# Kernel tuning notes

Measured on AMD Instinct MI355X. Metric: run time of the kernel, lower is better.

## Reference

```python
import jax, jax.numpy as jnp
import numpy as np

B, VH, VL, EP = 4, 130, 120, 256
DIN, DEP, D, H, NL = 256, 128, 512, 16, 8
HID = 4 * D

def _pe(x, base=1000.0):
    # sinusoidal positional encoding (base=1000 as in the module)
    L, Dm = x.shape[-2], x.shape[-1]
    pos = jnp.arange(L, dtype=jnp.float32)
    ch = jnp.arange(Dm, dtype=jnp.float32)
    ang = pos[:, None] / (base ** (2.0 * ch / ch[-1]))[None]
    enc = jnp.where(ch % 2 == 0, jnp.sin(ang), jnp.cos(ang))
    return x + enc

def _ln(x, g, b):
    m = x.mean(-1, keepdims=True)
    v = ((x - m) ** 2).mean(-1, keepdims=True)
    return (x - m) / jnp.sqrt(v + 1e-5) * g + b

def _gmha(x, rots, trans, mask_bias, qkv_w, out_w, out_b, g, b, r_s, d_s):
    # ESM3 geometric multi-head attention (algorithm 6)
    xn = _ln(x, g, b)
    qkv = (xn @ qkv_w.T).reshape(x.shape[0], x.shape[1], 5, H, 3)  # [B,L,5,H,3]
    qkv = jnp.einsum('brid,brfhd->brfhi', rots, qkv)               # rotate into global frame
    Qr, Kr, Qd, Kd, V = (qkv[..., f, :, :] for f in range(5))
    scale = 3.0 ** -0.5
    Ar = jnp.einsum('bihd,bjhd->bijh', Qr, Kr) * jax.nn.softplus(r_s) * scale
    qd = Qd + trans[:, :, None, :]
    kd = Kd + trans[:, :, None, :]
    dist = jnp.linalg.norm(qd[:, :, None] - kd[:, None], axis=-1)  # [B,i,j,H]
    logits = Ar - dist * jax.nn.softplus(d_s) * scale + mask_bias[..., None]
    A = jax.nn.softmax(logits, axis=2)
    o = jnp.einsum('bijh,bjhd->bihd', A, V)
    o = jnp.einsum('brji,brhj->brhi', rots, o)                     # rotate back (R^T)
    return o.reshape(x.shape[0], x.shape[1], H * 3) @ out_w.T + out_b

def _swiglu(x, g, b, w12, w3):
    # SwiGLU transition (dropout is identity in eval)
    h = _ln(x, g, b) @ w12.T
    a, v = jnp.split(h, 2, axis=-1)
    return (jax.nn.silu(a) * v) @ w3.T

def _forward(vh_x, vl_x, vh_rots, vh_trans, vl_rots, vl_trans, ep_feats, ep_rots, ep_trans,
             vh_emb_w, vl_emb_w, tgt_emb_w, qkv_w, out_w, out_b, ln_g, ln_b, r_scale, d_scale,
             ln2_g, ln2_b, w12, w3, out_vh_w, out_vh_gate_w, out_vh_gate_b,
             out_vl_w, out_vl_gate_w, out_vl_gate_b, vh_mask, vl_mask, ep_mask):
    emb = jnp.concatenate([_pe(vh_x @ vh_emb_w.T), _pe(vl_x @ vl_emb_w.T), ep_feats @ tgt_emb_w.T], axis=1)
    rots = jnp.concatenate([vh_rots, vl_rots, ep_rots], axis=1)
    trans = jnp.concatenate([vh_trans, vl_trans, ep_trans], axis=1)
    mask = jnp.concatenate([vh_mask, vl_mask, ep_mask], axis=1)
    mask_bias = jnp.where(mask[:, :, None] | mask[:, None, :], -1e9, 0.0)
    for i in range(NL):
        emb = emb + _gmha(emb, rots, trans, mask_bias, qkv_w[i], out_w[i], out_b[i],
                          ln_g[i], ln_b[i], r_scale[i], d_scale[i])
        emb = emb + _swiglu(emb, ln2_g[i], ln2_b[i], w12[i], w3[i])
    vh_e, vl_e = emb[:, :VH], emb[:, VH:VH + VL]
    vh_upd = (vh_e @ out_vh_w.T) * jax.nn.sigmoid(vh_e @ out_vh_gate_w.T + out_vh_gate_b)
    vl_upd = (vl_e @ out_vl_w.T) * jax.nn.sigmoid(vl_e @ out_vl_gate_w.T + out_vl_gate_b)
    vh_out = jnp.where(~vh_mask[..., None], vh_x + vh_upd, vh_x)
    vl_out = jnp.where(~vl_mask[..., None], vl_x + vl_upd, vl_x)
    return vh_out, vl_out

def setup_inputs():
    key = jax.random.key(0)
    ks = iter(jax.random.split(key, 40))
    s = 0.02
    return dict(
        vh_x=jax.random.normal(next(ks), (B, VH, DIN)),
        vl_x=jax.random.normal(next(ks), (B, VL, DIN)),
        vh_rots=jax.random.normal(next(ks), (B, VH, 3, 3)),
        vh_trans=jax.random.normal(next(ks), (B, VH, 3)),
        vl_rots=jax.random.normal(next(ks), (B, VL, 3, 3)),
        vl_trans=jax.random.normal(next(ks), (B, VL, 3)),
        ep_feats=jax.random.normal(next(ks), (B, EP, DEP)),
        ep_rots=jax.random.normal(next(ks), (B, EP, 3, 3)),
        ep_trans=jax.random.normal(next(ks), (B, EP, 3)),
        vh_mask=jnp.zeros((B, VH), dtype=bool),
        vl_mask=jnp.zeros((B, VL), dtype=bool),
        ep_mask=jax.random.randint(next(ks), (B, EP), 0, 2).astype(bool),
        vh_emb_w=jax.random.normal(next(ks), (D, DIN)) * s,
        vl_emb_w=jax.random.normal(next(ks), (D, DIN)) * s,
        tgt_emb_w=jax.random.normal(next(ks), (D, DEP)) * s,
        qkv_w=jax.random.normal(next(ks), (NL, H * 15, D)) * s,
        out_w=jax.random.normal(next(ks), (NL, D, H * 3)) * s,
        out_b=jnp.zeros((NL, D)),
        ln_g=jnp.ones((NL, D)), ln_b=jnp.zeros((NL, D)),
        r_scale=jnp.zeros((NL, H)), d_scale=jnp.zeros((NL, H)),
        ln2_g=jnp.ones((NL, D)), ln2_b=jnp.zeros((NL, D)),
        w12=jax.random.normal(next(ks), (NL, 2 * HID, D)) * s,
        w3=jax.random.normal(next(ks), (NL, D, HID)) * s,
        out_vh_w=jax.random.normal(next(ks), (DIN, D)) * s,
        out_vh_gate_w=jax.random.normal(next(ks), (DIN, D)) * s,
        out_vh_gate_b=jnp.full((DIN,), -2.0),
        out_vl_w=jax.random.normal(next(ks), (DIN, D)) * s,
        out_vl_gate_w=jax.random.normal(next(ks), (DIN, D)) * s,
        out_vl_gate_b=jnp.full((DIN,), -2.0),
    )

def reference(vh_x, vl_x, vh_rots, vh_trans, vl_rots, vl_trans, ep_feats, ep_rots, ep_trans,
              vh_mask, vl_mask, ep_mask,
              vh_emb_w, vl_emb_w, tgt_emb_w, qkv_w, out_w, out_b, ln_g, ln_b, r_scale, d_scale,
              ln2_g, ln2_b, w12, w3, out_vh_w, out_vh_gate_w, out_vh_gate_b,
              out_vl_w, out_vl_gate_w, out_vl_gate_b):
    return _forward(vh_x, vl_x, vh_rots, vh_trans, vl_rots, vl_trans, ep_feats, ep_rots, ep_trans,
                    vh_emb_w, vl_emb_w, tgt_emb_w, qkv_w, out_w, out_b, ln_g, ln_b, r_scale, d_scale,
                    ln2_g, ln2_b, w12, w3, out_vh_w, out_vh_gate_w, out_vh_gate_b,
                    out_vl_w, out_vl_gate_w, out_vl_gate_b, vh_mask, vl_mask, ep_mask)
```

## Files before the change

### kernel.cpp

```cpp
#include <hip/hip_runtime.h>
#include <hip/hip_bf16.h>
#include <math.h>
#include <stdint.h>

#define B_ 4
#define VH_ 130
#define VL_ 120
#define EP_ 256
#define R_ 506
#define RP_ 512
#define DIN_ 256
#define DEP_ 128
#define D_ 512
#define H_ 16
#define NL_ 8
#define HID_ 2048

#define MODE_STORE 0
#define MODE_ADD_BIAS 1

typedef _Float16 half8 __attribute__((ext_vector_type(8)));
typedef float f32x4 __attribute__((ext_vector_type(4)));

#define ASYNC16(ldsdst, gsrc)                                                  \
  __builtin_amdgcn_global_load_lds(                                            \
      (const __attribute__((address_space(1))) unsigned int*)(gsrc),           \
      (__attribute__((address_space(3))) unsigned int*)(ldsdst), 16, 0, 0)

__global__ __launch_bounds__(256) void gemm16sw_kernel(
    const _Float16* __restrict__ A, const _Float16* __restrict__ Wa,
    const _Float16* __restrict__ Wv, _Float16* __restrict__ Gh,
    int M, int K) {
  __shared__ _Float16 Al[4][4096];
  __shared__ _Float16 Ba[4][2048];
  __shared__ _Float16 Bv[4][2048];

  const int t = threadIdx.x;
  const int nbm = (M + 127) >> 7;
  const int nwg = gridDim.x;
  int bid = blockIdx.x;
  if ((nwg & 7) == 0) {
    int q = nwg >> 3;
    bid = (bid & 7) * q + (bid >> 3);
  }
  const int bm = bid % nbm, bn = bid / nbm;
  const int lane = t & 63;
  const int w = t >> 6;
  const int wm = w >> 1, wn = w & 1;

  const int r0 = t >> 2;
  const int cp = t & 3;
  const int gc = cp ^ ((r0 >> 1) & 3);
  int gr0 = bm * 128 + r0;       if (gr0 >= M) gr0 = M - 1;
  int gr1 = bm * 128 + 64 + r0;  if (gr1 >= M) gr1 = M - 1;
  const int gcol = bn * 64 + r0;
  const _Float16* pA0 = A + (size_t)gr0 * K + gc * 8;
  const _Float16* pA1 = A + (size_t)gr1 * K + gc * 8;
  const _Float16* pBa = Wa + (size_t)gcol * K + gc * 8;
  const _Float16* pBv = Wv + (size_t)gcol * K + gc * 8;

#define STAGE(buf, kt)                                                         \
  do {                                                                         \
    ASYNC16(&Al[buf][t * 8], pA0 + (size_t)(kt) * 32);                         \
    ASYNC16(&Al[buf][2048 + t * 8], pA1 + (size_t)(kt) * 32);                  \
    ASYNC16(&Ba[buf][t * 8], pBa + (size_t)(kt) * 32);                         \
    ASYNC16(&Bv[buf][t * 8], pBv + (size_t)(kt) * 32);                         \
  } while (0)

  f32x4 aca[4][2], acv[4][2];
#pragma unroll
  for (int i = 0; i < 4; i++)
#pragma unroll
    for (int j = 0; j < 2; j++) {
      aca[i][j] = (f32x4){0.f, 0.f, 0.f, 0.f};
      acv[i][j] = (f32x4){0.f, 0.f, 0.f, 0.f};
    }

  const int nt = K >> 5;
  STAGE(0, 0); STAGE(1, 1); STAGE(2, 2);

  const int rl = lane & 15;
  const int ca = (lane >> 4) ^ ((rl >> 1) & 3);
  for (int kt = 0; kt < nt; ++kt) {
    if (kt < nt - 2)       asm volatile("s_waitcnt vmcnt(8)" ::: "memory");
    else if (kt == nt - 2) asm volatile("s_waitcnt vmcnt(4)" ::: "memory");
    else                   asm volatile("s_waitcnt vmcnt(0)" ::: "memory");
    __builtin_amdgcn_s_barrier();
    const int buf = kt & 3;
    const _Float16* Ab  = &Al[buf][(wm * 64 + rl) * 32 + ca * 8];
    const _Float16* Bab = &Ba[buf][(wn * 32 + rl) * 32 + ca * 8];
    const _Float16* Bvb = &Bv[buf][(wn * 32 + rl) * 32 + ca * 8];
    half8 af[4], bfa[2], bfv[2];
#pragma unroll
    for (int i = 0; i < 4; i++) af[i] = *(const half8*)(Ab + i * 512);
#pragma unroll
    for (int j = 0; j < 2; j++) {
      bfa[j] = *(const half8*)(Bab + j * 512);
      bfv[j] = *(const half8*)(Bvb + j * 512);
    }
#pragma unroll
    for (int i = 0; i < 4; i++)
#pragma unroll
      for (int j = 0; j < 2; j++) {
        aca[i][j] = __builtin_amdgcn_mfma_f32_16x16x32_f16(af[i], bfa[j],
                                                           aca[i][j], 0, 0, 0);
        acv[i][j] = __builtin_amdgcn_mfma_f32_16x16x32_f16(af[i], bfv[j],
                                                           acv[i][j], 0, 0, 0);
      }
    if (kt + 3 < nt) STAGE((kt + 3) & 3, kt + 3);
  }
#undef STAGE

  const int rb = bm * 128 + wm * 64 + ((lane >> 4) << 2);
  const int cb = bn * 64 + wn * 32 + (lane & 15);
#pragma unroll
  for (int i = 0; i < 4; i++) {
#pragma unroll
    for (int j = 0; j < 2; j++) {
      int col = cb + j * 16;
#pragma unroll
      for (int q = 0; q < 4; q++) {
        int row = rb + i * 16 + q;
        if (row >= M) continue;
        float a = aca[i][j][q];
        float v = acv[i][j][q];
        Gh[(size_t)row * HID_ + col] = (_Float16)((a / (1.f + expf(-a))) * v);
      }
    }
  }
}

__global__ __launch_bounds__(256) void gemm16b_kernel(
    const _Float16* __restrict__ A, const _Float16* __restrict__ W,
    float* __restrict__ C, const float* __restrict__ bias,
    int M, int N, int K, int mode, int crpb, int cR, int cbase, int pe) {
  __shared__ _Float16 Al[4][2048];
  __shared__ _Float16 Bl[4][2048];

  const int t = threadIdx.x;
  const int nbm = (M + 63) >> 6;
  const int nwg = gridDim.x;
  int bid = blockIdx.x;
  if ((nwg & 7) == 0) {
    int q = nwg >> 3;
    bid = (bid & 7) * q + (bid >> 3);
  }
  const int bm = bid % nbm, bn = bid / nbm;
  const int lane = t & 63;
  const int w = t >> 6;
  const int wm = w >> 1, wn = w & 1;

  const int r0 = t >> 2;
  const int cp = t & 3;
  const int gc = cp ^ ((r0 >> 1) & 3);
  int gr = bm * 64 + r0;    if (gr >= M) gr = M - 1;
  int gcol = bn * 64 + r0;  if (gcol >= N) gcol = N - 1;
  const _Float16* pA = A + (size_t)gr * K + gc * 8;
  const _Float16* pB = W + (size_t)gcol * K + gc * 8;

#define STAGE(buf, kt)                                                         \
  do {                                                                         \
    ASYNC16(&Al[buf][t * 8], pA + (size_t)(kt) * 32);                          \
    ASYNC16(&Bl[buf][t * 8], pB + (size_t)(kt) * 32);                          \
  } while (0)

  f32x4 acc[2][2];
#pragma unroll
  for (int i = 0; i < 2; i++)
#pragma unroll
    for (int j = 0; j < 2; j++) acc[i][j] = (f32x4){0.f, 0.f, 0.f, 0.f};

  const int nt = K >> 5;
  STAGE(0, 0); STAGE(1, 1); STAGE(2, 2);

  const int rl = lane & 15;
  const int ca = (lane >> 4) ^ ((rl >> 1) & 3);
  for (int kt = 0; kt < nt; ++kt) {
    if (kt < nt - 2)       asm volatile("s_waitcnt vmcnt(4)" ::: "memory");
    else if (kt == nt - 2) asm volatile("s_waitcnt vmcnt(2)" ::: "memory");
    else                   asm volatile("s_waitcnt vmcnt(0)" ::: "memory");
    __builtin_amdgcn_s_barrier();
    const int buf = kt & 3;
    half8 af[2], bf[2];
#pragma unroll
    for (int i = 0; i < 2; i++)
      af[i] = *(const half8*)&Al[buf][(wm * 32 + i * 16 + rl) * 32 + ca * 8];
#pragma unroll
    for (int j = 0; j < 2; j++)
      bf[j] = *(const half8*)&Bl[buf][(wn * 32 + j * 16 + rl) * 32 + ca * 8];
#pragma unroll
    for (int i = 0; i < 2; i++)
#pragma unroll
      for (int j = 0; j < 2; j++)
        acc[i][j] = __builtin_amdgcn_mfma_f32_16x16x32_f16(af[i], bf[j],
                                                           acc[i][j], 0, 0, 0);
    if (kt + 3 < nt) STAGE((kt + 3) & 3, kt + 3);
  }
#undef STAGE

  const float PEK = -0.02703623196464017f;
  const int rb = bm * 64 + wm * 32 + ((lane >> 4) << 2);
  const int cb = bn * 64 + wn * 32 + (lane & 15);
#pragma unroll
  for (int i = 0; i < 2; i++) {
#pragma unroll
    for (int j = 0; j < 2; j++) {
      int col = cb + j * 16;
      if (col >= N) continue;
#pragma unroll
      for (int q = 0; q < 4; q++) {
        int row = rb + i * 16 + q;
        if (row >= M) continue;
        int crow = (row / crpb) * cR + cbase + row % crpb;
        size_t idx = (size_t)crow * N + col;
        float v = acc[i][j][q];
        if (pe) {
          float pos = (float)(row % crpb);
          float ang = pos * expf((float)col * PEK);
          v += (col & 1) ? cosf(ang) : sinf(ang);
        }
        if (mode == MODE_STORE) C[idx] = v;
        else {
          float bb = bias ? bias[col] : 0.f;
          C[idx] = C[idx] + v + bb;
        }
      }
    }
  }
}

__global__ __launch_bounds__(256) void gemm16gate_kernel(
    const _Float16* __restrict__ A, const _Float16* __restrict__ Wv,
    const _Float16* __restrict__ Wg, const float* __restrict__ x,
    const float* __restrict__ gb, const int* __restrict__ mask,
    float* __restrict__ out, int M, int K, int arpb, int aR, int abase) {
  __shared__ _Float16 Al[4][2048];
  __shared__ _Float16 Bva[4][2048];
  __shared__ _Float16 Bga[4][2048];

  const int t = threadIdx.x;
  const int nbm = (M + 63) >> 6;
  const int nwg = gridDim.x;
  int bid = blockIdx.x;
  if ((nwg & 7) == 0) {
    int q = nwg >> 3;
    bid = (bid & 7) * q + (bid >> 3);
  }
  const int bm = bid % nbm, bn = bid / nbm;
  const int lane = t & 63;
  const int w = t >> 6;
  const int wm = w >> 1, wn = w & 1;

  const int r0 = t >> 2;
  const int cp = t & 3;
  const int gc = cp ^ ((r0 >> 1) & 3);
  int gr = bm * 64 + r0;  if (gr >= M) gr = M - 1;
  int ar = (gr / arpb) * aR + abase + gr % arpb;
  const int gcol = bn * 64 + r0;
  const _Float16* pA  = A + (size_t)ar * K + gc * 8;
  const _Float16* pBv = Wv + (size_t)gcol * K + gc * 8;
  const _Float16* pBg = Wg + (size_t)gcol * K + gc * 8;

#define STAGE(buf, kt)                                                         \
  do {                                                                         \
    ASYNC16(&Al[buf][t * 8], pA + (size_t)(kt) * 32);                          \
    ASYNC16(&Bva[buf][t * 8], pBv + (size_t)(kt) * 32);                        \
    ASYNC16(&Bga[buf][t * 8], pBg + (size_t)(kt) * 32);                        \
  } while (0)

  f32x4 acv[2][2], acg[2][2];
#pragma unroll
  for (int i = 0; i < 2; i++)
#pragma unroll
    for (int j = 0; j < 2; j++) {
      acv[i][j] = (f32x4){0.f, 0.f, 0.f, 0.f};
      acg[i][j] = (f32x4){0.f, 0.f, 0.f, 0.f};
    }

  const int nt = K >> 5;
  STAGE(0, 0); STAGE(1, 1); STAGE(2, 2);

  const int rl = lane & 15;
  const int ca = (lane >> 4) ^ ((rl >> 1) & 3);
  for (int kt = 0; kt < nt; ++kt) {
    if (kt < nt - 2)       asm volatile("s_waitcnt vmcnt(6)" ::: "memory");
    else if (kt == nt - 2) asm volatile("s_waitcnt vmcnt(3)" ::: "memory");
    else                   asm volatile("s_waitcnt vmcnt(0)" ::: "memory");
    __builtin_amdgcn_s_barrier();
    const int buf = kt & 3;
    half8 af[2], bv[2], bg2[2];
#pragma unroll
    for (int i = 0; i < 2; i++)
      af[i] = *(const half8*)&Al[buf][(wm * 32 + i * 16 + rl) * 32 + ca * 8];
#pragma unroll
    for (int j = 0; j < 2; j++) {
      bv[j] = *(const half8*)&Bva[buf][(wn * 32 + j * 16 + rl) * 32 + ca * 8];
      bg2[j] = *(const half8*)&Bga[buf][(wn * 32 + j * 16 + rl) * 32 + ca * 8];
    }
#pragma unroll
    for (int i = 0; i < 2; i++)
#pragma unroll
      for (int j = 0; j < 2; j++) {
        acv[i][j] = __builtin_amdgcn_mfma_f32_16x16x32_f16(af[i], bv[j],
                                                           acv[i][j], 0, 0, 0);
        acg[i][j] = __builtin_amdgcn_mfma_f32_16x16x32_f16(af[i], bg2[j],
                                                           acg[i][j], 0, 0, 0);
      }
    if (kt + 3 < nt) STAGE((kt + 3) & 3, kt + 3);
  }
#undef STAGE

  const int rb = bm * 64 + wm * 32 + ((lane >> 4) << 2);
  const int cb = bn * 64 + wn * 32 + (lane & 15);
#pragma unroll
  for (int i = 0; i < 2; i++) {
#pragma unroll
    for (int j = 0; j < 2; j++) {
      int col = cb + j * 16;
#pragma unroll
      for (int q = 0; q < 4; q++) {
        int row = rb + i * 16 + q;
        if (row >= M) continue;
        size_t idx = (size_t)row * DIN_ + col;
        float xv = x[idx];
        float res;
        if (mask[row]) {
          res = xv;
        } else {
          float gate = 1.f / (1.f + expf(-(acg[i][j][q] + gb[col])));
          res = xv + acv[i][j][q] * gate;
        }
        out[idx] = res;
      }
    }
  }
}

__global__ __launch_bounds__(256) void ln_kernel(
    const float* __restrict__ x, const float* __restrict__ g,
    const float* __restrict__ b, _Float16* __restrict__ out) {
  const int row = blockIdx.x;
  const int t = threadIdx.x;
  const float* xr = x + (size_t)row * D_;
  float v0 = xr[t], v1 = xr[t + 256];
  float s = v0 + v1, s2 = v0 * v0 + v1 * v1;
#pragma unroll
  for (int o = 32; o > 0; o >>= 1) {
    s += __shfl_down(s, o);
    s2 += __shfl_down(s2, o);
  }
  __shared__ float w1[4], w2[4], mv[2];
  const int w = t >> 6;
  if ((t & 63) == 0) { w1[w] = s; w2[w] = s2; }
  __syncthreads();
  if (t == 0) {
    float ss = w1[0] + w1[1] + w1[2] + w1[3];
    float ss2 = w2[0] + w2[1] + w2[2] + w2[3];
    float mean = ss * (1.f / D_);
    float var = ss2 * (1.f / D_) - mean * mean;
    mv[0] = mean;
    mv[1] = rsqrtf(var + 1e-5f);
  }
  __syncthreads();
  float mean = mv[0], inv = mv[1];
  _Float16* orow = out + (size_t)row * D_;
  orow[t] = (_Float16)((v0 - mean) * inv * g[t] + b[t]);
  orow[t + 256] = (_Float16)((v1 - mean) * inv * g[t + 256] + b[t + 256]);
}

struct ThSegs {
  const float* src[13];
  _Float16* dst[13];
  int cum[14];
};
__global__ void tohalf_multi_kernel(ThSegs sg) {
  int total = sg.cum[13];
  for (int i = blockIdx.x * blockDim.x + threadIdx.x; i < total;
       i += gridDim.x * blockDim.x) {
    int s = 0;
    while (i >= sg.cum[s + 1]) s++;
    int off = i - sg.cum[s];
    const float4* p = (const float4*)(sg.src[s] + (size_t)off * 16);
    float4 x = p[0], y = p[1], z = p[2], w = p[3];
    half8 h0 = {(_Float16)x.x, (_Float16)x.y, (_Float16)x.z, (_Float16)x.w,
                (_Float16)y.x, (_Float16)y.y, (_Float16)y.z, (_Float16)y.w};
    half8 h1 = {(_Float16)z.x, (_Float16)z.y, (_Float16)z.z, (_Float16)z.w,
                (_Float16)w.x, (_Float16)w.y, (_Float16)w.z, (_Float16)w.w};
    half8* d = (half8*)(sg.dst[s] + (size_t)off * 16);
    d[0] = h0;
    d[1] = h1;
  }
}

__global__ void tohalf_kernel(const float* __restrict__ src,
                              _Float16* __restrict__ dst, int n8) {
  for (int i = blockIdx.x * blockDim.x + threadIdx.x; i < n8;
       i += gridDim.x * blockDim.x) {
    const float4* s = (const float4*)(src + (size_t)i * 8);
    float4 x = s[0], y = s[1];
    half8 h = {(_Float16)x.x, (_Float16)x.y, (_Float16)x.z, (_Float16)x.w,
               (_Float16)y.x, (_Float16)y.y, (_Float16)y.z, (_Float16)y.w};
    *(half8*)(dst + (size_t)i * 8) = h;
  }
}

__global__ void transpose_ow_kernel(const float* __restrict__ out_w,
                                    float* __restrict__ owT) {
  int idx = blockIdx.x * blockDim.x + threadIdx.x;
  const int total = NL_ * 48 * D_;
  if (idx >= total) return;
  int l = idx / (48 * D_);
  int rem = idx % (48 * D_);
  int k = rem / D_;
  int c = rem % D_;
  owT[idx] = out_w[(size_t)l * D_ * 48 + (size_t)c * 48 + k];
}

__global__ void prep_kernel(
    const float* __restrict__ vh_rots, const float* __restrict__ vh_trans,
    const float* __restrict__ vl_rots, const float* __restrict__ vl_trans,
    const float* __restrict__ ep_rots, const float* __restrict__ ep_trans,
    const int* __restrict__ vh_mask, const int* __restrict__ vl_mask,
    const int* __restrict__ ep_mask, float* __restrict__ rots,
    float* __restrict__ trans, int* __restrict__ mask,
    int* __restrict__ maskp, float* __restrict__ Kt, float* __restrict__ PKt,
    float* __restrict__ Vt) {
  int idx = blockIdx.x * blockDim.x + threadIdx.x;
  if (idx < B_ * RP_) {
    int b = idx >> 9, r = idx & (RP_ - 1);
    if (r >= R_) {
      maskp[idx] = 1;
      return;
    }
    const float* sr; const float* st; int sm;
    if (r < VH_) {
      sr = vh_rots + (size_t)(b * VH_ + r) * 9;
      st = vh_trans + (size_t)(b * VH_ + r) * 3;
      sm = vh_mask[b * VH_ + r];
    } else if (r < VH_ + VL_) {
      int rr = r - VH_;
      sr = vl_rots + (size_t)(b * VL_ + rr) * 9;
      st = vl_trans + (size_t)(b * VL_ + rr) * 3;
      sm = vl_mask[b * VL_ + rr];
    } else {
      int rr = r - VH_ - VL_;
      sr = ep_rots + (size_t)(b * EP_ + rr) * 9;
      st = ep_trans + (size_t)(b * EP_ + rr) * 3;
      sm = ep_mask[b * EP_ + rr];
    }
    int lin = b * R_ + r;
    maskp[idx] = sm;
    mask[lin] = sm;
#pragma unroll
    for (int k = 0; k < 9; k++) rots[(size_t)lin * 9 + k] = sr[k];
#pragma unroll
    for (int k = 0; k < 3; k++) trans[(size_t)lin * 3 + k] = st[k];
  } else {
    int p = idx - B_ * RP_;
    const int per = B_ * H_ * (RP_ - R_) * 4;
    if (p >= 3 * per) return;
    int a = p / per;
    int q = p % per;
    int bh = q / ((RP_ - R_) * 4);
    int rem = q % ((RP_ - R_) * 4);
    float* dst = (a == 0) ? Kt : (a == 1) ? PKt : Vt;
    dst[(size_t)bh * RP_ * 4 + (size_t)R_ * 4 + rem] = 0.f;
  }
}

__global__ __launch_bounds__(128) void rotate_kernel(
    const float* __restrict__ qkv_raw, const float* __restrict__ rots,
    const float* __restrict__ trans, float* __restrict__ Qrow,
    float* __restrict__ PQrow, float* __restrict__ Kt,
    float* __restrict__ PKt, float* __restrict__ Vt) {
  const int blk = blockIdx.x;
  const int b = blk / R_;
  const int r = blk % R_;
  const int t = threadIdx.x;
  __shared__ float Rm[9], tr[3], raw[240];
  if (t < 9) Rm[t] = rots[(size_t)blk * 9 + t];
  if (t >= 9 && t < 12) tr[t - 9] = trans[(size_t)blk * 3 + (t - 9)];
  for (int i = t; i < 240; i += 128) raw[i] = qkv_raw[(size_t)blk * 240 + i];
  __syncthreads();
  if (t < 80) {
    int f = t / 16, h = t % 16;
    float x = raw[f * 48 + h * 3 + 0];
    float y = raw[f * 48 + h * 3 + 1];
    float z = raw[f * 48 + h * 3 + 2];
    float r0 = Rm[0] * x + Rm[1] * y + Rm[2] * z;
    float r1 = Rm[3] * x + Rm[4] * y + Rm[5] * z;
    float r2 = Rm[6] * x + Rm[7] * y + Rm[8] * z;
    if (f == 2 || f == 3) { r0 += tr[0]; r1 += tr[1]; r2 += tr[2]; }
    if (f == 0 || f == 2) {
      float* dst = (f == 0) ? Qrow : PQrow;
      size_t o = (size_t)blk * 48 + h * 3;
      dst[o] = r0; dst[o + 1] = r1; dst[o + 2] = r2;
    } else {
      float* dst = (f == 1) ? Kt : (f == 3) ? PKt : Vt;
      size_t base = ((size_t)(b * H_ + h) * RP_ + r) * 4;
      *(float4*)(dst + base) = make_float4(r0, r1, r2, 0.f);
    }
  }
}

__global__ __launch_bounds__(256) void attn2_kernel(
    const float* __restrict__ Qrow, const float* __restrict__ PQrow,
    const float* __restrict__ Kt, const float* __restrict__ PKt,
    const float* __restrict__ Vt, const float* __restrict__ rots,
    const int* __restrict__ mask, const int* __restrict__ maskp,
    const float* __restrict__ rs, const float* __restrict__ ds,
    const float* __restrict__ owT, const float* __restrict__ out_b,
    float* __restrict__ emb) {
  const int blk = blockIdx.x;
  const int b = blk / (R_ / 2);
  const int ip = blk % (R_ / 2);
  const int i0 = ip * 2;
  const int t = threadIdx.x;
  const int lane = t & 63;
  const int w = t >> 6;

  __shared__ float qs[2][48], ps[2][48], og[2][48];
  __shared__ float crs[16], cds[16];
  __shared__ int mi[2];

  if (t < 96) {
    int io = t / 48, k2 = t % 48;
    int i = i0 + io;
    qs[io][k2] = Qrow[((size_t)(b * R_ + i)) * 48 + k2];
    ps[io][k2] = PQrow[((size_t)(b * R_ + i)) * 48 + k2];
  } else if (t < 112) {
    int h = t - 96;
    const float sc = 0.57735026918962576f;
    crs[h] = log1pf(expf(rs[h])) * sc;
    cds[h] = log1pf(expf(ds[h])) * sc;
  } else if (t < 114) {
    mi[t - 112] = mask[b * R_ + i0 + (t - 112)];
  }
  __syncthreads();

  float mb[8];
#pragma unroll
  for (int jb = 0; jb < 8; jb++) {
    int j = jb * 64 + lane;
    mb[jb] = maskp[b * RP_ + j] ? -1e9f : 0.f;
  }
  const float bi0 = mi[0] ? -1e9f : 0.f;
  const float bi1 = mi[1] ? -1e9f : 0.f;

  for (int hh = 0; hh < 4; hh++) {
    const int h = hh * 4 + w;
    const float sA = crs[h], sD = cds[h];
    const float qx0 = qs[0][h * 3], qy0 = qs[0][h * 3 + 1], qz0 = qs[0][h * 3 + 2];
    const float px0 = ps[0][h * 3], py0 = ps[0][h * 3 + 1], pz0 = ps[0][h * 3 + 2];
    const float qx1 = qs[1][h * 3], qy1 = qs[1][h * 3 + 1], qz1 = qs[1][h * 3 + 2];
    const float px1 = ps[1][h * 3], py1 = ps[1][h * 3 + 1], pz1 = ps[1][h * 3 + 2];
    const float4* kb4 = (const float4*)(Kt + ((size_t)(b * H_ + h) * RP_) * 4);
    const float4* pb4 = (const float4*)(PKt + ((size_t)(b * H_ + h) * RP_) * 4);
    const float4* vb4 = (const float4*)(Vt + ((size_t)(b * H_ + h) * RP_) * 4);

    float l0[8], l1[8];
    float m0 = -3e38f, m1 = -3e38f;
#pragma unroll
    for (int jb = 0; jb < 8; jb++) {
      int j = jb * 64 + lane;
      float4 k4 = kb4[j];
      float4 p4 = pb4[j];
      float dx0 = px0 - p4.x, dy0 = py0 - p4.y, dz0 = pz0 - p4.z;
      float d0 = sqrtf(dx0 * dx0 + dy0 * dy0 + dz0 * dz0);
      l0[jb] = (qx0 * k4.x + qy0 * k4.y + qz0 * k4.z) * sA - d0 * sD + mb[jb] + bi0;
      m0 = fmaxf(m0, l0[jb]);
      float dx1 = px1 - p4.x, dy1 = py1 - p4.y, dz1 = pz1 - p4.z;
      float d1 = sqrtf(dx1 * dx1 + dy1 * dy1 + dz1 * dz1);
      l1[jb] = (qx1 * k4.x + qy1 * k4.y + qz1 * k4.z) * sA - d1 * sD + mb[jb] + bi1;
      m1 = fmaxf(m1, l1[jb]);
    }
#pragma unroll
    for (int s = 1; s < 64; s <<= 1) {
      m0 = fmaxf(m0, __shfl_xor(m0, s));
      m1 = fmaxf(m1, __shfl_xor(m1, s));
    }
    float s0 = 0.f, s1 = 0.f;
    float ox0 = 0.f, oy0 = 0.f, oz0 = 0.f, ox1 = 0.f, oy1 = 0.f, oz1 = 0.f;
#pragma unroll
    for (int jb = 0; jb < 8; jb++) {
      int j = jb * 64 + lane;
      float p0 = expf(l0[jb] - m0);
      float p1 = expf(l1[jb] - m1);
      s0 += p0; s1 += p1;
      float4 v4 = vb4[j];
      ox0 += p0 * v4.x; oy0 += p0 * v4.y; oz0 += p0 * v4.z;
      ox1 += p1 * v4.x; oy1 += p1 * v4.y; oz1 += p1 * v4.z;
    }
#pragma unroll
    for (int s = 1; s < 64; s <<= 1) {
      s0 += __shfl_xor(s0, s); s1 += __shfl_xor(s1, s);
      ox0 += __shfl_xor(ox0, s); oy0 += __shfl_xor(oy0, s); oz0 += __shfl_xor(oz0, s);
      ox1 += __shfl_xor(ox1, s); oy1 += __shfl_xor(oy1, s); oz1 += __shfl_xor(oz1, s);
    }
    if (lane == 0) {
      og[0][h * 3] = ox0 / s0; og[0][h * 3 + 1] = oy0 / s0; og[0][h * 3 + 2] = oz0 / s0;
      og[1][h * 3] = ox1 / s1; og[1][h * 3 + 1] = oy1 / s1; og[1][h * 3 + 2] = oz1 / s1;
    }
  }
  __syncthreads();
  float r0v0 = 0.f, r0v1 = 0.f;
  if (t < 48) {
    int hh = t / 3, i3 = t % 3;
    const float* Rm0 = rots + ((size_t)(b * R_ + i0)) * 9;
    const float* Rm1 = rots + ((size_t)(b * R_ + i0 + 1)) * 9;
    r0v0 = Rm0[0 + i3] * og[0][hh * 3 + 0] + Rm0[3 + i3] * og[0][hh * 3 + 1] +
           Rm0[6 + i3] * og[0][hh * 3 + 2];
    r0v1 = Rm1[0 + i3] * og[1][hh * 3 + 0] + Rm1[3 + i3] * og[1][hh * 3 + 1] +
           Rm1[6 + i3] * og[1][hh * 3 + 2];
  }
  __syncthreads();
  if (t < 48) { og[0][t] = r0v0; og[1][t] = r0v1; }
  __syncthreads();
#pragma unroll
  for (int io = 0; io < 2; io++) {
    float* erow = emb + ((size_t)(b * R_ + i0 + io)) * D_;
#pragma unroll
    for (int half = 0; half < 2; half++) {
      int c = half * 256 + t;
      float a0 = 0.f, a1 = 0.f, a2 = 0.f, a3 = 0.f;
#pragma unroll
      for (int k = 0; k < 48; k += 4) {
        a0 += og[io][k + 0] * owT[(size_t)(k + 0) * D_ + c];
        a1 += og[io][k + 1] * owT[(size_t)(k + 1) * D_ + c];
        a2 += og[io][k + 2] * owT[(size_t)(k + 2) * D_ + c];
        a3 += og[io][k + 3] * owT[(size_t)(k + 3) * D_ + c];
      }
      erow[c] += out_b[c] + ((a0 + a1) + (a2 + a3));
    }
  }
}

extern "C" void kernel_launch(void* const* d_in, const int* in_sizes, int n_in,
                              void* d_out, int out_size, void* d_ws, size_t ws_size,
                              hipStream_t stream) {
  const float* vh_x = (const float*)d_in[0];
  const float* vl_x = (const float*)d_in[1];
  const float* vh_rots = (const float*)d_in[2];
  const float* vh_trans = (const float*)d_in[3];
  const float* vl_rots = (const float*)d_in[4];
  const float* vl_trans = (const float*)d_in[5];
  const float* ep_feats = (const float*)d_in[6];
  const float* ep_rots = (const float*)d_in[7];
  const float* ep_trans = (const float*)d_in[8];
  const int* vh_mask = (const int*)d_in[9];
  const int* vl_mask = (const int*)d_in[10];
  const int* ep_mask = (const int*)d_in[11];
  const float* vh_emb_w = (const float*)d_in[12];
  const float* vl_emb_w = (const float*)d_in[13];
  const float* tgt_emb_w = (const float*)d_in[14];
  const float* qkv_w = (const float*)d_in[15];
  const float* out_w = (const float*)d_in[16];
  const float* out_b = (const float*)d_in[17];
  const float* ln_g = (const float*)d_in[18];
  const float* ln_b = (const float*)d_in[19];
  const float* r_scale = (const float*)d_in[20];
  const float* d_scale = (const float*)d_in[21];
  const float* ln2_g = (const float*)d_in[22];
  const float* ln2_b = (const float*)d_in[23];
  const float* w12 = (const float*)d_in[24];
  const float* w3 = (const float*)d_in[25];
  const float* out_vh_w = (const float*)d_in[26];
  const float* out_vh_gate_w = (const float*)d_in[27];
  const float* out_vh_gate_b = (const float*)d_in[28];
  const float* out_vl_w = (const float*)d_in[29];
  const float* out_vl_gate_w = (const float*)d_in[30];
  const float* out_vl_gate_b = (const float*)d_in[31];

  const int BR = B_ * R_;

  uint8_t* P = (uint8_t*)d_ws;
  auto alloc = [&](size_t bytes) {
    uint8_t* p = P;
    P += (bytes + 255) & ~(size_t)255;
    return p;
  };
  float* emb = (float*)alloc((size_t)BR * D_ * 4);
  _Float16* xnh = (_Float16*)alloc((size_t)BR * D_ * 2);
  float* qkvr = (float*)alloc((size_t)BR * 240 * 4);
  float* Qrow = (float*)alloc((size_t)BR * 48 * 4);
  float* PQrow = (float*)alloc((size_t)BR * 48 * 4);
  float* Kt = (float*)alloc((size_t)B_ * H_ * RP_ * 4 * 4);
  float* PKt = (float*)alloc((size_t)B_ * H_ * RP_ * 4 * 4);
  float* Vt = (float*)alloc((size_t)B_ * H_ * RP_ * 4 * 4);
  _Float16* ghalf = (_Float16*)alloc((size_t)BR * HID_ * 2);
  float* rots_c = (float*)alloc((size_t)BR * 9 * 4);
  float* trans_c = (float*)alloc((size_t)BR * 3 * 4);
  int* mask_c = (int*)alloc((size_t)BR * 4);
  int* maskp = (int*)alloc((size_t)B_ * RP_ * 4);
  float* owT = (float*)alloc((size_t)NL_ * 48 * D_ * 4);
  _Float16* embh = (_Float16*)alloc((size_t)BR * D_ * 2);
  _Float16* qkvh = (_Float16*)alloc((size_t)NL_ * 240 * D_ * 2);
  _Float16* w12h = (_Float16*)alloc((size_t)NL_ * 2 * HID_ * D_ * 2);
  _Float16* w3h = (_Float16*)alloc((size_t)NL_ * D_ * HID_ * 2);
  _Float16* vhxh = (_Float16*)alloc((size_t)B_ * VH_ * DIN_ * 2);
  _Float16* vlxh = (_Float16*)alloc((size_t)B_ * VL_ * DIN_ * 2);
  _Float16* eph = (_Float16*)alloc((size_t)B_ * EP_ * DEP_ * 2);
  _Float16* vhewh = (_Float16*)alloc((size_t)D_ * DIN_ * 2);
  _Float16* vlewh = (_Float16*)alloc((size_t)D_ * DIN_ * 2);
  _Float16* tgewh = (_Float16*)alloc((size_t)D_ * DEP_ * 2);
  _Float16* ovhw = (_Float16*)alloc((size_t)DIN_ * D_ * 2);
  _Float16* ovhgw = (_Float16*)alloc((size_t)DIN_ * D_ * 2);
  _Float16* ovlw = (_Float16*)alloc((size_t)DIN_ * D_ * 2);
  _Float16* ovlgw = (_Float16*)alloc((size_t)DIN_ * D_ * 2);

  {
    ThSegs sg;
    const float* srcs[13] = {qkv_w, w12, w3, vh_x, vl_x, ep_feats,
                             vh_emb_w, vl_emb_w, tgt_emb_w,
                             out_vh_w, out_vh_gate_w, out_vl_w, out_vl_gate_w};
    _Float16* dsts[13] = {qkvh, w12h, w3h, vhxh, vlxh, eph,
                          vhewh, vlewh, tgewh, ovhw, ovhgw, ovlw, ovlgw};
    int n16s[13] = {NL_ * 240 * D_ / 16, NL_ * 2 * HID_ * D_ / 16,
                    NL_ * D_ * HID_ / 16, B_ * VH_ * DIN_ / 16,
                    B_ * VL_ * DIN_ / 16, B_ * EP_ * DEP_ / 16,
                    D_ * DIN_ / 16, D_ * DIN_ / 16, D_ * DEP_ / 16,
                    DIN_ * D_ / 16, DIN_ * D_ / 16, DIN_ * D_ / 16,
                    DIN_ * D_ / 16};
    int c = 0;
    for (int i = 0; i < 13; i++) {
      sg.src[i] = srcs[i]; sg.dst[i] = dsts[i];
      sg.cum[i] = c; c += n16s[i];
    }
    sg.cum[13] = c;
    tohalf_multi_kernel<<<2048, 256, 0, stream>>>(sg);
  }

  {
    int total = NL_ * 48 * D_;
    transpose_ow_kernel<<<(total + 255) / 256, 256, 0, stream>>>(out_w, owT);
  }

  {
    int total = B_ * RP_ + 3 * B_ * H_ * (RP_ - R_) * 4;
    prep_kernel<<<(total + 255) / 256, 256, 0, stream>>>(
        vh_rots, vh_trans, vl_rots, vl_trans, ep_rots, ep_trans, vh_mask,
        vl_mask, ep_mask, rots_c, trans_c, mask_c, maskp, Kt, PKt, Vt);
  }

  auto gemm16b = [&](const _Float16* A, const _Float16* W, float* C,
                     const float* bias, int M, int N, int K, int mode,
                     int crpb, int cR, int cbase, int pe) {
    int nbm = (M + 63) / 64, nbn = (N + 63) / 64;
    gemm16b_kernel<<<nbm * nbn, 256, 0, stream>>>(A, W, C, bias, M, N, K, mode,
                                                  crpb, cR, cbase, pe);
  };

  gemm16b(vhxh, vhewh, emb, nullptr, B_ * VH_, D_, DIN_, MODE_STORE,
          VH_, R_, 0, 1);
  gemm16b(vlxh, vlewh, emb, nullptr, B_ * VL_, D_, DIN_, MODE_STORE,
          VL_, R_, VH_, 1);
  gemm16b(eph, tgewh, emb, nullptr, B_ * EP_, D_, DEP_, MODE_STORE,
          EP_, R_, VH_ + VL_, 0);

  for (int l = 0; l < NL_; l++) {
    const _Float16* qwh = qkvh + (size_t)l * 240 * D_;
    const float* owTl = owT + (size_t)l * 48 * D_;
    const float* obias = out_b + (size_t)l * D_;
    const float* lg = ln_g + (size_t)l * D_;
    const float* lb = ln_b + (size_t)l * D_;
    const float* l2g = ln2_g + (size_t)l * D_;
    const float* l2b = ln2_b + (size_t)l * D_;
    const float* rs = r_scale + (size_t)l * H_;
    const float* dsc = d_scale + (size_t)l * H_;
    const _Float16* w12ah = w12h + (size_t)l * 2 * HID_ * D_;
    const _Float16* w12bh = w12ah + (size_t)HID_ * D_;
    const _Float16* w3lh = w3h + (size_t)l * D_ * HID_;

    ln_kernel<<<BR, 256, 0, stream>>>(emb, lg, lb, xnh);
    gemm16b(xnh, qwh, qkvr, nullptr, BR, 240, D_, MODE_STORE, BR, BR, 0, 0);
    rotate_kernel<<<BR, 128, 0, stream>>>(qkvr, rots_c, trans_c, Qrow, PQrow,
                                          Kt, PKt, Vt);
    attn2_kernel<<<B_ * (R_ / 2), 256, 0, stream>>>(
        Qrow, PQrow, Kt, PKt, Vt, rots_c, mask_c, maskp, rs, dsc, owTl, obias,
        emb);

    ln_kernel<<<BR, 256, 0, stream>>>(emb, l2g, l2b, xnh);
    {
      int nbm = (BR + 127) / 128, nbn = HID_ / 64;
      gemm16sw_kernel<<<nbm * nbn, 256, 0, stream>>>(xnh, w12ah, w12bh, ghalf,
                                                     BR, D_);
    }
    gemm16b(ghalf, w3lh, emb, nullptr, BR, D_, HID_, MODE_ADD_BIAS,
            BR, BR, 0, 0);
  }

  tohalf_kernel<<<1024, 256, 0, stream>>>(emb, embh, BR * D_ / 8);
  {
    int M = B_ * VH_;
    int nbm = (M + 63) / 64;
    gemm16gate_kernel<<<nbm * 4, 256, 0, stream>>>(
        embh, ovhw, ovhgw, vh_x, out_vh_gate_b, vh_mask, (float*)d_out, M, D_,
        VH_, R_, 0);
  }
  {
    int M = B_ * VL_;
    int nbm = (M + 63) / 64;
    gemm16gate_kernel<<<nbm * 4, 256, 0, stream>>>(
        embh, ovlw, ovlgw, vl_x, out_vl_gate_b, vl_mask,
        (float*)d_out + (size_t)B_ * VH_ * DIN_, M, D_, VL_, R_, VH_);
  }
}
```

Baseline: 1.083 ms.

## Process four query rows per attention block and fuse post-attention LayerNorm

The geometric attention kernel now handles four query rows per block instead of two, so each K/PK/V load and each output-projection weight load is reused across more rows. The second LayerNorm is folded into the attention epilogue, which removes one kernel launch and a full re-read of the embedding per layer. The fp16 conversion kernel switches from a grid-stride loop to a one-thread-per-chunk launch. In exchange the attention kernel uses more registers, launches half as many blocks, clamps its padded tail rows, and adds per-row block barriers for the LayerNorm reduction.

New measurement: 1.278 ms. 1.18x slower.

```diff
diff --git a/kernel.cpp b/kernel.cpp
--- a/kernel.cpp
+++ b/kernel.cpp
@@ -9,6 +9,7 @@
 #define EP_ 256
 #define R_ 506
 #define RP_ 512
+#define NPB_ 127
 #define DIN_ 256
 #define DEP_ 128
 #define D_ 512
@@ -373,23 +374,21 @@
   _Float16* dst[13];
   int cum[14];
 };
-__global__ void tohalf_multi_kernel(ThSegs sg) {
-  int total = sg.cum[13];
-  for (int i = blockIdx.x * blockDim.x + threadIdx.x; i < total;
-       i += gridDim.x * blockDim.x) {
-    int s = 0;
-    while (i >= sg.cum[s + 1]) s++;
-    int off = i - sg.cum[s];
-    const float4* p = (const float4*)(sg.src[s] + (size_t)off * 16);
-    float4 x = p[0], y = p[1], z = p[2], w = p[3];
-    half8 h0 = {(_Float16)x.x, (_Float16)x.y, (_Float16)x.z, (_Float16)x.w,
-                (_Float16)y.x, (_Float16)y.y, (_Float16)y.z, (_Float16)y.w};
-    half8 h1 = {(_Float16)z.x, (_Float16)z.y, (_Float16)z.z, (_Float16)z.w,
-                (_Float16)w.x, (_Float16)w.y, (_Float16)w.z, (_Float16)w.w};
-    half8* d = (half8*)(sg.dst[s] + (size_t)off * 16);
-    d[0] = h0;
-    d[1] = h1;
-  }
+__global__ void tohalf_multi_kernel(ThSegs sg, int total) {
+  int i = blockIdx.x * blockDim.x + threadIdx.x;
+  if (i >= total) return;
+  int s = 0;
+  while (i >= sg.cum[s + 1]) s++;
+  int off = i - sg.cum[s];
+  const float4* p = (const float4*)(sg.src[s] + (size_t)off * 16);
+  float4 x = p[0], y = p[1], z = p[2], w = p[3];
+  half8 h0 = {(_Float16)x.x, (_Float16)x.y, (_Float16)x.z, (_Float16)x.w,
+              (_Float16)y.x, (_Float16)y.y, (_Float16)y.z, (_Float16)y.w};
+  half8 h1 = {(_Float16)z.x, (_Float16)z.y, (_Float16)z.z, (_Float16)z.w,
+              (_Float16)w.x, (_Float16)w.y, (_Float16)w.z, (_Float16)w.w};
+  half8* d = (half8*)(sg.dst[s] + (size_t)off * 16);
+  d[0] = h0;
+  d[1] = h1;
 }
 
 __global__ void tohalf_kernel(const float* __restrict__ src,
@@ -510,31 +509,35 @@
     const int* __restrict__ mask, const int* __restrict__ maskp,
     const float* __restrict__ rs, const float* __restrict__ ds,
     const float* __restrict__ owT, const float* __restrict__ out_b,
-    float* __restrict__ emb) {
+    const float* __restrict__ l2g, const float* __restrict__ l2b,
+    float* __restrict__ emb, _Float16* __restrict__ xnh) {
   const int blk = blockIdx.x;
-  const int b = blk / (R_ / 2);
-  const int ip = blk % (R_ / 2);
-  const int i0 = ip * 2;
+  const int b = blk / NPB_;
+  const int ip = blk % NPB_;
+  const int i0 = ip * 4;
   const int t = threadIdx.x;
   const int lane = t & 63;
   const int w = t >> 6;
 
-  __shared__ float qs[2][48], ps[2][48], og[2][48];
+  __shared__ float qs[4][48], ps[4][48], og[4][48];
   __shared__ float crs[16], cds[16];
-  __shared__ int mi[2];
-
-  if (t < 96) {
+  __shared__ int mi[4];
+  __shared__ float lw[4], lw2[4], mv2[2];
+
+  if (t < 192) {
     int io = t / 48, k2 = t % 48;
-    int i = i0 + io;
+    int i = i0 + io; if (i >= R_) i = R_ - 1;
     qs[io][k2] = Qrow[((size_t)(b * R_ + i)) * 48 + k2];
     ps[io][k2] = PQrow[((size_t)(b * R_ + i)) * 48 + k2];
-  } else if (t < 112) {
-    int h = t - 96;
+  } else if (t < 208) {
+    int h = t - 192;
     const float sc = 0.57735026918962576f;
     crs[h] = log1pf(expf(rs[h])) * sc;
     cds[h] = log1pf(expf(ds[h])) * sc;
-  } else if (t < 114) {
-    mi[t - 112] = mask[b * R_ + i0 + (t - 112)];
+  } else if (t < 212) {
+    int io = t - 208;
+    int i = i0 + io; if (i >= R_) i = R_ - 1;
+    mi[io] = mask[b * R_ + i];
   }
   __syncthreads();
 
@@ -544,94 +547,142 @@
     int j = jb * 64 + lane;
     mb[jb] = maskp[b * RP_ + j] ? -1e9f : 0.f;
   }
-  const float bi0 = mi[0] ? -1e9f : 0.f;
-  const float bi1 = mi[1] ? -1e9f : 0.f;
+  float bi[4];
+#pragma unroll
+  for (int io = 0; io < 4; io++) bi[io] = mi[io] ? -1e9f : 0.f;
 
   for (int hh = 0; hh < 4; hh++) {
     const int h = hh * 4 + w;
     const float sA = crs[h], sD = cds[h];
-    const float qx0 = qs[0][h * 3], qy0 = qs[0][h * 3 + 1], qz0 = qs[0][h * 3 + 2];
-    const float px0 = ps[0][h * 3], py0 = ps[0][h * 3 + 1], pz0 = ps[0][h * 3 + 2];
-    const float qx1 = qs[1][h * 3], qy1 = qs[1][h * 3 + 1], qz1 = qs[1][h * 3 + 2];
-    const float px1 = ps[1][h * 3], py1 = ps[1][h * 3 + 1], pz1 = ps[1][h * 3 + 2];
+    float qx[4], qy[4], qz[4], px[4], py[4], pz[4];
+#pragma unroll
+    for (int io = 0; io < 4; io++) {
+      qx[io] = qs[io][h * 3]; qy[io] = qs[io][h * 3 + 1]; qz[io] = qs[io][h * 3 + 2];
+      px[io] = ps[io][h * 3]; py[io] = ps[io][h * 3 + 1]; pz[io] = ps[io][h * 3 + 2];
+    }
     const float4* kb4 = (const float4*)(Kt + ((size_t)(b * H_ + h) * RP_) * 4);
     const float4* pb4 = (const float4*)(PKt + ((size_t)(b * H_ + h) * RP_) * 4);
     const float4* vb4 = (const float4*)(Vt + ((size_t)(b * H_ + h) * RP_) * 4);
 
-    float l0[8], l1[8];
-    float m0 = -3e38f, m1 = -3e38f;
+    float l[4][8];
+    float m[4] = {-3e38f, -3e38f, -3e38f, -3e38f};
 #pragma unroll
     for (int jb = 0; jb < 8; jb++) {
       int j = jb * 64 + lane;
       float4 k4 = kb4[j];
       float4 p4 = pb4[j];
-      float dx0 = px0 - p4.x, dy0 = py0 - p4.y, dz0 = pz0 - p4.z;
-      float d0 = sqrtf(dx0 * dx0 + dy0 * dy0 + dz0 * dz0);
-      l0[jb] = (qx0 * k4.x + qy0 * k4.y + qz0 * k4.z) * sA - d0 * sD + mb[jb] + bi0;
-      m0 = fmaxf(m0, l0[jb]);
-      float dx1 = px1 - p4.x, dy1 = py1 - p4.y, dz1 = pz1 - p4.z;
-      float d1 = sqrtf(dx1 * dx1 + dy1 * dy1 + dz1 * dz1);
-      l1[jb] = (qx1 * k4.x + qy1 * k4.y + qz1 * k4.z) * sA - d1 * sD + mb[jb] + bi1;
-      m1 = fmaxf(m1, l1[jb]);
-    }
-#pragma unroll
-    for (int s = 1; s < 64; s <<= 1) {
-      m0 = fmaxf(m0, __shfl_xor(m0, s));
-      m1 = fmaxf(m1, __shfl_xor(m1, s));
-    }
-    float s0 = 0.f, s1 = 0.f;
-    float ox0 = 0.f, oy0 = 0.f, oz0 = 0.f, ox1 = 0.f, oy1 = 0.f, oz1 = 0.f;
+#pragma unroll
+      for (int io = 0; io < 4; io++) {
+        float dx = px[io] - p4.x, dy = py[io] - p4.y, dz = pz[io] - p4.z;
+        float d = sqrtf(dx * dx + dy * dy + dz * dz);
+        l[io][jb] = (qx[io] * k4.x + qy[io] * k4.y + qz[io] * k4.z) * sA -
+                    d * sD + mb[jb] + bi[io];
+        m[io] = fmaxf(m[io], l[io][jb]);
+      }
+    }
+#pragma unroll
+    for (int s = 1; s < 64; s <<= 1)
+#pragma unroll
+      for (int io = 0; io < 4; io++) m[io] = fmaxf(m[io], __shfl_xor(m[io], s));
+
+    float sm[4] = {0.f, 0.f, 0.f, 0.f};
+    float ox[4] = {0.f, 0.f, 0.f, 0.f};
+    float oy[4] = {0.f, 0.f, 0.f, 0.f};
+    float oz[4] = {0.f, 0.f, 0.f, 0.f};
 #pragma unroll
     for (int jb = 0; jb < 8; jb++) {
       int j = jb * 64 + lane;
-      float p0 = expf(l0[jb] - m0);
-      float p1 = expf(l1[jb] - m1);
-      s0 += p0; s1 += p1;
       float4 v4 = vb4[j];
-      ox0 += p0 * v4.x; oy0 += p0 * v4.y; oz0 += p0 * v4.z;
-      ox1 += p1 * v4.x; oy1 += p1 * v4.y; oz1 += p1 * v4.z;
-    }
-#pragma unroll
-    for (int s = 1; s < 64; s <<= 1) {
-      s0 += __shfl_xor(s0, s); s1 += __shfl_xor(s1, s);
-      ox0 += __shfl_xor(ox0, s); oy0 += __shfl_xor(oy0, s); oz0 += __shfl_xor(oz0, s);
-      ox1 += __shfl_xor(ox1, s); oy1 += __shfl_xor(oy1, s); oz1 += __shfl_xor(oz1, s);
-    }
+#pragma unroll
+      for (int io = 0; io < 4; io++) {
+        float p = expf(l[io][jb] - m[io]);
+        sm[io] += p;
+        ox[io] += p * v4.x; oy[io] += p * v4.y; oz[io] += p * v4.z;
+      }
+    }
+#pragma unroll
+    for (int s = 1; s < 64; s <<= 1)
+#pragma unroll
+      for (int io = 0; io < 4; io++) {
+        sm[io] += __shfl_xor(sm[io], s);
+        ox[io] += __shfl_xor(ox[io], s);
+        oy[io] += __shfl_xor(oy[io], s);
+        oz[io] += __shfl_xor(oz[io], s);
+      }
     if (lane == 0) {
-      og[0][h * 3] = ox0 / s0; og[0][h * 3 + 1] = oy0 / s0; og[0][h * 3 + 2] = oz0 / s0;
-      og[1][h * 3] = ox1 / s1; og[1][h * 3 + 1] = oy1 / s1; og[1][h * 3 + 2] = oz1 / s1;
+#pragma unroll
+      for (int io = 0; io < 4; io++) {
+        og[io][h * 3] = ox[io] / sm[io];
+        og[io][h * 3 + 1] = oy[io] / sm[io];
+        og[io][h * 3 + 2] = oz[io] / sm[io];
+      }
     }
   }
   __syncthreads();
-  float r0v0 = 0.f, r0v1 = 0.f;
+  float rv[4] = {0.f, 0.f, 0.f, 0.f};
   if (t < 48) {
     int hh = t / 3, i3 = t % 3;
-    const float* Rm0 = rots + ((size_t)(b * R_ + i0)) * 9;
-    const float* Rm1 = rots + ((size_t)(b * R_ + i0 + 1)) * 9;
-    r0v0 = Rm0[0 + i3] * og[0][hh * 3 + 0] + Rm0[3 + i3] * og[0][hh * 3 + 1] +
-           Rm0[6 + i3] * og[0][hh * 3 + 2];
-    r0v1 = Rm1[0 + i3] * og[1][hh * 3 + 0] + Rm1[3 + i3] * og[1][hh * 3 + 1] +
-           Rm1[6 + i3] * og[1][hh * 3 + 2];
+#pragma unroll
+    for (int io = 0; io < 4; io++) {
+      int i = i0 + io; if (i >= R_) i = R_ - 1;
+      const float* Rm = rots + ((size_t)(b * R_ + i)) * 9;
+      rv[io] = Rm[0 + i3] * og[io][hh * 3 + 0] +
+               Rm[3 + i3] * og[io][hh * 3 + 1] +
+               Rm[6 + i3] * og[io][hh * 3 + 2];
+    }
   }
   __syncthreads();
-  if (t < 48) { og[0][t] = r0v0; og[1][t] = r0v1; }
+  if (t < 48) {
+#pragma unroll
+    for (int io = 0; io < 4; io++) og[io][t] = rv[io];
+  }
   __syncthreads();
-#pragma unroll
-  for (int io = 0; io < 2; io++) {
-    float* erow = emb + ((size_t)(b * R_ + i0 + io)) * D_;
-#pragma unroll
-    for (int half = 0; half < 2; half++) {
-      int c = half * 256 + t;
-      float a0 = 0.f, a1 = 0.f, a2 = 0.f, a3 = 0.f;
-#pragma unroll
-      for (int k = 0; k < 48; k += 4) {
-        a0 += og[io][k + 0] * owT[(size_t)(k + 0) * D_ + c];
-        a1 += og[io][k + 1] * owT[(size_t)(k + 1) * D_ + c];
-        a2 += og[io][k + 2] * owT[(size_t)(k + 2) * D_ + c];
-        a3 += og[io][k + 3] * owT[(size_t)(k + 3) * D_ + c];
-      }
-      erow[c] += out_b[c] + ((a0 + a1) + (a2 + a3));
-    }
+
+  const int c0 = t, c1 = t + 256;
+  float pj0[4] = {0.f, 0.f, 0.f, 0.f};
+  float pj1[4] = {0.f, 0.f, 0.f, 0.f};
+#pragma unroll
+  for (int k = 0; k < 48; k++) {
+    float w0 = owT[(size_t)k * D_ + c0];
+    float w1 = owT[(size_t)k * D_ + c1];
+#pragma unroll
+    for (int io = 0; io < 4; io++) {
+      pj0[io] += og[io][k] * w0;
+      pj1[io] += og[io][k] * w1;
+    }
+  }
+  const float ob0 = out_b[c0], ob1 = out_b[c1];
+
+#pragma unroll
+  for (int io = 0; io < 4; io++) {
+    if (i0 + io >= R_) continue;
+    const size_t row = (size_t)(b * R_ + i0 + io);
+    float* erow = emb + row * D_;
+    float val0 = erow[c0] + ob0 + pj0[io];
+    float val1 = erow[c1] + ob1 + pj1[io];
+    erow[c0] = val0;
+    erow[c1] = val1;
+    float s = val0 + val1, s2 = val0 * val0 + val1 * val1;
+#pragma unroll
+    for (int o = 32; o > 0; o >>= 1) {
+      s += __shfl_down(s, o);
+      s2 += __shfl_down(s2, o);
+    }
+    if ((t & 63) == 0) { lw[w] = s; lw2[w] = s2; }
+    __syncthreads();
+    if (t == 0) {
+      float ss = lw[0] + lw[1] + lw[2] + lw[3];
+      float ss2 = lw2[0] + lw2[1] + lw2[2] + lw2[3];
+      float mean = ss * (1.f / D_);
+      float var = ss2 * (1.f / D_) - mean * mean;
+      mv2[0] = mean;
+      mv2[1] = rsqrtf(var + 1e-5f);
+    }
+    __syncthreads();
+    float mean = mv2[0], inv = mv2[1];
+    _Float16* xr = xnh + row * D_;
+    xr[c0] = (_Float16)((val0 - mean) * inv * l2g[c0] + l2b[c0]);
+    xr[c1] = (_Float16)((val1 - mean) * inv * l2g[c1] + l2b[c1]);
   }
 }
 
@@ -727,7 +778,7 @@
       sg.cum[i] = c; c += n16s[i];
     }
     sg.cum[13] = c;
-    tohalf_multi_kernel<<<2048, 256, 0, stream>>>(sg);
+    tohalf_multi_kernel<<<(c + 255) / 256, 256, 0, stream>>>(sg, c);
   }
 
   {
@@ -775,11 +826,10 @@
     gemm16b(xnh, qwh, qkvr, nullptr, BR, 240, D_, MODE_STORE, BR, BR, 0, 0);
     rotate_kernel<<<BR, 128, 0, stream>>>(qkvr, rots_c, trans_c, Qrow, PQrow,
                                           Kt, PKt, Vt);
-    attn2_kernel<<<B_ * (R_ / 2), 256, 0, stream>>>(
+    attn2_kernel<<<B_ * NPB_, 256, 0, stream>>>(
         Qrow, PQrow, Kt, PKt, Vt, rots_c, mask_c, maskp, rs, dsc, owTl, obias,
-        emb);
-
-    ln_kernel<<<BR, 256, 0, stream>>>(emb, l2g, l2b, xnh);
+        l2g, l2b, emb, xnh);
+
     {
       int nbm = (BR + 127) / 128, nbn = HID_ / 64;
       gemm16sw_kernel<<<nbm * nbn, 256, 0, stream>>>(xnh, w12ah, w12bh, ghalf,
```
